# Performance work log

Hardware: AMD Instinct MI355X
Metric: run time of the kernel (lower is better)

The kernel has to match this reference:

```python
import jax, jax.numpy as jnp
import numpy as np

N, C, L, D, F = 8, 128, 512, 64, 512
ATTN_W = 64
LN_EPS = 1e-5
ATTN_EPS = 1e-6


def _xavier(k, shape):
    lim = float(np.sqrt(6.0 / (shape[0] + shape[1])))
    return jax.random.uniform(k, shape, jnp.float32, -lim, lim)


def setup_inputs() -> dict:
    key = jax.random.key(0)
    ks = jax.random.split(key, 8)
    return dict(
        x=jax.random.normal(ks[0], (N, C, L), jnp.float32),
        Wx=_xavier(ks[1], (C, D)),
        Wt=_xavier(ks[2], (C, D)),
        bh=jnp.zeros((D,), jnp.float32),
        Wa=_xavier(ks[3], (D, 1)),
        ba=jnp.zeros((1,), jnp.float32),
        W0=_xavier(ks[4], (C, F)),
        b0=jnp.zeros((F,), jnp.float32),
        W1=_xavier(ks[5], (F, C)),
        b1=jnp.zeros((C,), jnp.float32),
        g0=jnp.ones((C,), jnp.float32),
        be0=jnp.zeros((C,), jnp.float32),
        g1=jnp.ones((C,), jnp.float32),
        be1=jnp.zeros((C,), jnp.float32),
    )


def _layernorm(y, g, b):
    mu = jnp.mean(y, axis=-1, keepdims=True)
    var = jnp.var(y, axis=-1, keepdims=True)
    return (y - mu) * jax.lax.rsqrt(var + LN_EPS) * g + b


def reference(x, Wx, Wt, bh, Wa, ba, W0, b0, W1, b1, g0, be0, g1, be1):
    xt = jnp.transpose(x, (0, 2, 1))  # (N, L, C)
    q = jnp.einsum('nlc,cd->nld', xt, Wt)  # (N, L, D)
    k = jnp.einsum('nlc,cd->nld', xt, Wx)  # (N, L, D)
    # additive (Bahdanau) scores: h is the large (N, L, L, D) intermediate
    h = jnp.tanh(q[:, :, None, :] + k[:, None, :, :] + bh)
    e = jnp.einsum('nlmd,d->nlm', h, Wa[:, 0]) + ba[0]  # (N, L, L)
    e = jnp.exp(e - jnp.max(e, axis=-1, keepdims=True))
    # local band mask: tril(w//2 - 1) & triu(-w//2) on (row i, col j)
    dij = jnp.arange(L)[None, :] - jnp.arange(L)[:, None]  # j - i
    mask = (dij <= ATTN_W // 2 - 1) & (dij >= -(ATTN_W // 2))
    e = jnp.where(mask, e, 0.0)
    a = e / (jnp.sum(e, axis=-1, keepdims=True) + ATTN_EPS)  # (N, L, L)
    v = jnp.einsum('nlm,nmc->nlc', a, xt)  # (N, L, C)
    x2 = _layernorm(v + xt, g0, be0)
    x3 = jnp.einsum('nlf,fc->nlc', jax.nn.relu(jnp.einsum('nlc,cf->nlf', x2, W0) + b0), W1) + b1
    x4 = _layernorm(x3 + x2, g1, be1)
    return (jnp.transpose(x4, (0, 2, 1)), a)
```

## Files before the change

kernel.cpp:

```cpp
#include <hip/hip_runtime.h>
#include <cstddef>


__global__ __launch_bounds__(512) void prep_kernel(
    const float* __restrict__ x, const float* __restrict__ Wt,
    const float* __restrict__ Wx, float* __restrict__ q,
    float* __restrict__ k) {
  __shared__ float xs[128][17];
  int tid = threadIdx.x;
  int n = blockIdx.x >> 5;
  int l0 = (blockIdx.x & 31) << 4;

  {
    int c = tid >> 2, v = tid & 3;
    float4 d4 = *(const float4*)(x + ((size_t)n * 128 + c) * 512 + l0 + 4 * v);
    xs[c][4 * v + 0] = d4.x; xs[c][4 * v + 1] = d4.y;
    xs[c][4 * v + 2] = d4.z; xs[c][4 * v + 3] = d4.w;
  }
  __syncthreads();

  int half = tid >> 8;
  int t = tid & 255;
  int r = t >> 4;
  int f0 = (t & 15) << 2;
  const float* W = half ? Wx : Wt;
  float* dst = half ? k : q;
  float acc[4] = {0.f, 0.f, 0.f, 0.f};
#pragma unroll 4
  for (int cc = 0; cc < 128; cc++) {
    float xv = xs[cc][r];
    float4 w = *(const float4*)(W + cc * 64 + f0);
    acc[0] += xv * w.x; acc[1] += xv * w.y;
    acc[2] += xv * w.z; acc[3] += xv * w.w;
  }
  *(float4*)(dst + ((size_t)n * 512 + l0 + r) * 64 + f0) =
      make_float4(acc[0], acc[1], acc[2], acc[3]);
}

__global__ __launch_bounds__(512, 4) void attn_ffn_fused_kernel(
    const float* __restrict__ x, const float* __restrict__ q,
    const float* __restrict__ k, const float* __restrict__ bh,
    const float* __restrict__ Wa, const float* __restrict__ ba,
    const float* __restrict__ g0, const float* __restrict__ be0,
    const float* __restrict__ W0, const float* __restrict__ b0,
    const float* __restrict__ W1, const float* __restrict__ b1,
    const float* __restrict__ g1, const float* __restrict__ be1,
    float* __restrict__ a, float* __restrict__ out) {
  __shared__ __align__(16) char smem[61440];
  __shared__ __align__(16) float xstT[128][12];
  __shared__ __align__(16) float avT[71][10];
  __shared__ __align__(16) float was[64];

  float (*ks)[68] = (float(*)[68])smem;
  float (*qs)[64] = (float(*)[64])(smem + 19312);
  float (*xtw)[77] = (float(*)[77])(smem + 21360);
  float (*tstT)[12] = (float(*)[12])smem;
  float (*part)[8][128] = (float(*)[8][128])(smem + 24576);
  float (*ys)[128] = (float(*)[128])(smem + 57344);

  int tid = threadIdx.x;
  int w = tid >> 6, lane = tid & 63;
  int bid = blockIdx.x;
  int tile = (bid & 7) * 64 + (bid >> 3);
  size_t rbase = (size_t)tile * 8;
  int n = (int)(rbase >> 9);
  int i0 = (int)(rbase & 511);
  int jlo0 = i0 - 32;

  if (tid < 64) was[tid] = Wa[tid];
  for (int idx = tid; idx < 71 * 10; idx += 512) ((float*)avT)[idx] = 0.f;
  if (tid < 128) {
    int r = tid >> 4, d4 = (tid & 15) << 2;
    float4 qv = *(const float4*)(q + ((size_t)n * 512 + i0 + r) * 64 + d4);
    float4 bv = *(const float4*)(bh + d4);
    *(float4*)(&qs[r][d4]) =
        make_float4(qv.x + bv.x, qv.y + bv.y, qv.z + bv.z, qv.w + bv.w);
  }
  for (int idx = tid; idx < 71 * 16; idx += 512) {
    int row = idx >> 4, d4 = (idx & 15) << 2;
    int j = jlo0 + row;
    float4 v = make_float4(0.f, 0.f, 0.f, 0.f);
    if (j >= 0 && j < 512)
      v = *(const float4*)(k + ((size_t)n * 512 + j) * 64 + d4);
    *(float4*)(&ks[row][d4]) = v;
  }
  for (int t = tid; t < 128 * 18; t += 512) {
    int c = t / 18;
    int u = t - c * 18;
    int col = 4 * u;
    int j0 = jlo0 + col;
    const float* xp = x + ((size_t)n * 128 + c) * 512;
    float4 v = make_float4(0.f, 0.f, 0.f, 0.f);
    if (j0 >= 0 && j0 + 3 < 512) {
      v = *(const float4*)(xp + j0);
    } else {
      if (j0 + 0 >= 0 && j0 + 0 < 512) v.x = xp[j0 + 0];
      if (j0 + 1 >= 0 && j0 + 1 < 512) v.y = xp[j0 + 1];
      if (j0 + 2 >= 0 && j0 + 2 < 512) v.z = xp[j0 + 2];
      if (j0 + 3 >= 0 && j0 + 3 < 512) v.w = xp[j0 + 3];
    }
    xtw[c][col + 0] = v.x; xtw[c][col + 1] = v.y;
    xtw[c][col + 2] = v.z; xtw[c][col + 3] = v.w;
  }
  __syncthreads();

  {
    int r = w;
    int i = i0 + r;
    int j = jlo0 + r + lane;
    bool valid = (j >= 0 && j < 512);
    const float* krow = &ks[r + lane][0];
    float e = 0.f;
#pragma unroll
    for (int d4 = 0; d4 < 64; d4 += 4) {
      float4 kv = *(const float4*)(krow + d4);
      float4 qv = *(const float4*)(&qs[r][d4]);
      float4 wv = *(const float4*)(&was[d4]);
      float h0 = qv.x + kv.x, h1 = qv.y + kv.y;
      float h2 = qv.z + kv.z, h3 = qv.w + kv.w;
      float t0 = 1.f - 2.f * __builtin_amdgcn_rcpf(__expf(2.f * h0) + 1.f);
      float t1 = 1.f - 2.f * __builtin_amdgcn_rcpf(__expf(2.f * h1) + 1.f);
      float t2 = 1.f - 2.f * __builtin_amdgcn_rcpf(__expf(2.f * h2) + 1.f);
      float t3 = 1.f - 2.f * __builtin_amdgcn_rcpf(__expf(2.f * h3) + 1.f);
      e += wv.x * t0 + wv.y * t1 + wv.z * t2 + wv.w * t3;
    }
    e += ba[0];
    if (!valid) e = -1e30f;

    float m = e;
    for (int o = 32; o > 0; o >>= 1) m = fmaxf(m, __shfl_xor(m, o, 64));
    float ex = valid ? __expf(e - m) : 0.f;
    float s = ex;
    for (int o = 32; o > 0; o >>= 1) s += __shfl_xor(s, o, 64);
    avT[r + lane][r] = ex / (s + 1e-6f);

    float* arow = a + ((size_t)n * 512 + i) * 512;
    int jlo = i - 32;
#pragma unroll
    for (int t = 0; t < 2; t++) {
      int col0 = 4 * lane + 256 * t;
      float4 v;
      { int jr = col0 + 0 - jlo; int jc = min(max(jr, 0), 63); v.x = (jr >= 0 && jr < 64) ? avT[r + jc][r] : 0.f; }
      { int jr = col0 + 1 - jlo; int jc = min(max(jr, 0), 63); v.y = (jr >= 0 && jr < 64) ? avT[r + jc][r] : 0.f; }
      { int jr = col0 + 2 - jlo; int jc = min(max(jr, 0), 63); v.z = (jr >= 0 && jr < 64) ? avT[r + jc][r] : 0.f; }
      { int jr = col0 + 3 - jlo; int jc = min(max(jr, 0), 63); v.w = (jr >= 0 && jr < 64) ? avT[r + jc][r] : 0.f; }
      *(float4*)(arow + col0) = v;
    }
  }
  __syncthreads();

  {
    int c = tid & 127;
    int r0 = (tid >> 7) << 1;
    const float* xr = &xtw[c][0];
    float acc0 = 0.f, acc1 = 0.f;
#pragma unroll 5
    for (int m = 0; m < 65; m++) {
      int col = r0 + m;
      float xv = xr[col];
      float2 av2 = *(const float2*)(&avT[col][r0]);
      acc0 += av2.x * xv;
      acc1 += av2.y * xv;
    }
    float res0 = xr[32 + r0];
    float res1 = xr[33 + r0];
    *(float2*)(&xstT[c][r0]) = make_float2(acc0 + res0, acc1 + res1);
  }
  __syncthreads();

  {
    float a0 = xstT[lane][w], a1 = xstT[lane + 64][w];
    float s = a0 + a1, s2 = a0 * a0 + a1 * a1;
    for (int o = 32; o > 0; o >>= 1) {
      s += __shfl_xor(s, o, 64);
      s2 += __shfl_xor(s2, o, 64);
    }
    float mu = s * (1.f / 128.f);
    float var = s2 * (1.f / 128.f) - mu * mu;
    float rs = rsqrtf(var + 1e-5f);
    xstT[lane][w] = (a0 - mu) * rs * g0[lane] + be0[lane];
    xstT[lane + 64][w] = (a1 - mu) * rs * g0[lane + 64] + be0[lane + 64];
  }
  __syncthreads();

  {
    int g = lane & 15;
    int kq = lane >> 4;
    int f0 = (16 * w + g) << 2;
    int ccb = kq << 5;
    const float* w0p = W0 + (size_t)ccb * 512 + f0;
    float acc[8][4];
#pragma unroll
    for (int i = 0; i < 8; i++)
#pragma unroll
      for (int u = 0; u < 4; u++) acc[i][u] = 0.f;

    float4 wbuf[4];
#pragma unroll
    for (int p = 0; p < 4; p++)
      wbuf[p] = *(const float4*)(w0p + (size_t)p * 512);
#pragma unroll
    for (int c4 = 0; c4 < 8; c4++) {
      float4 cur0 = wbuf[0], cur1 = wbuf[1], cur2 = wbuf[2], cur3 = wbuf[3];
      if (c4 < 7) {
#pragma unroll
        for (int p = 0; p < 4; p++)
          wbuf[p] = *(const float4*)(w0p + (size_t)((c4 + 1) * 4 + p) * 512);
      }
#pragma unroll
      for (int p = 0; p < 4; p++) {
        int cc = ccb + c4 * 4 + p;
        float4 wv = (p == 0) ? cur0 : (p == 1) ? cur1 : (p == 2) ? cur2 : cur3;
        float4 xa = *(const float4*)(&xstT[cc][0]);
        float4 xb = *(const float4*)(&xstT[cc][4]);
        acc[0][0] += xa.x * wv.x; acc[0][1] += xa.x * wv.y; acc[0][2] += xa.x * wv.z; acc[0][3] += xa.x * wv.w;
        acc[1][0] += xa.y * wv.x; acc[1][1] += xa.y * wv.y; acc[1][2] += xa.y * wv.z; acc[1][3] += xa.y * wv.w;
        acc[2][0] += xa.z * wv.x; acc[2][1] += xa.z * wv.y; acc[2][2] += xa.z * wv.z; acc[2][3] += xa.z * wv.w;
        acc[3][0] += xa.w * wv.x; acc[3][1] += xa.w * wv.y; acc[3][2] += xa.w * wv.z; acc[3][3] += xa.w * wv.w;
        acc[4][0] += xb.x * wv.x; acc[4][1] += xb.x * wv.y; acc[4][2] += xb.x * wv.z; acc[4][3] += xb.x * wv.w;
        acc[5][0] += xb.y * wv.x; acc[5][1] += xb.y * wv.y; acc[5][2] += xb.y * wv.z; acc[5][3] += xb.y * wv.w;
        acc[6][0] += xb.z * wv.x; acc[6][1] += xb.z * wv.y; acc[6][2] += xb.z * wv.z; acc[6][3] += xb.z * wv.w;
        acc[7][0] += xb.w * wv.x; acc[7][1] += xb.w * wv.y; acc[7][2] += xb.w * wv.z; acc[7][3] += xb.w * wv.w;
      }
    }
#pragma unroll
    for (int i = 0; i < 8; i++)
#pragma unroll
      for (int u = 0; u < 4; u++) {
        float v = acc[i][u];
        v += __shfl_xor(v, 16, 64);
        v += __shfl_xor(v, 32, 64);
        acc[i][u] = v;
      }
    int f = f0 + kq;
    float bb = b0[f];
    float r0v[8];
#pragma unroll
    for (int i = 0; i < 8; i++) {
      float v = (kq == 0) ? acc[i][0] : (kq == 1) ? acc[i][1]
              : (kq == 2) ? acc[i][2] : acc[i][3];
      r0v[i] = fmaxf(v + bb, 0.f);
    }
    *(float4*)(&tstT[f][0]) = make_float4(r0v[0], r0v[1], r0v[2], r0v[3]);
    *(float4*)(&tstT[f][4]) = make_float4(r0v[4], r0v[5], r0v[6], r0v[7]);
  }
  __syncthreads();

  {
    int c0 = (lane & 31) << 2;
    int rh = lane >> 5;
    const float* W1p = W1 + (size_t)w * 64 * 128 + c0;
    int tb = w << 6;
    float acc[4][4];
#pragma unroll
    for (int i = 0; i < 4; i++)
#pragma unroll
      for (int u = 0; u < 4; u++) acc[i][u] = 0.f;

    float4 wbuf[4];
#pragma unroll
    for (int p = 0; p < 4; p++)
      wbuf[p] = *(const float4*)(W1p + (size_t)p * 128);
#pragma unroll
    for (int t4 = 0; t4 < 16; t4++) {
      float4 cur0 = wbuf[0], cur1 = wbuf[1], cur2 = wbuf[2], cur3 = wbuf[3];
      if (t4 < 15) {
#pragma unroll
        for (int p = 0; p < 4; p++)
          wbuf[p] = *(const float4*)(W1p + (size_t)((t4 + 1) * 4 + p) * 128);
      }
#pragma unroll
      for (int p = 0; p < 4; p++) {
        int t = t4 * 4 + p;
        float4 wv = (p == 0) ? cur0 : (p == 1) ? cur1 : (p == 2) ? cur2 : cur3;
        float4 tv = *(const float4*)(&tstT[tb + t][4 * rh]);
        acc[0][0] += tv.x * wv.x; acc[0][1] += tv.x * wv.y; acc[0][2] += tv.x * wv.z; acc[0][3] += tv.x * wv.w;
        acc[1][0] += tv.y * wv.x; acc[1][1] += tv.y * wv.y; acc[1][2] += tv.y * wv.z; acc[1][3] += tv.y * wv.w;
        acc[2][0] += tv.z * wv.x; acc[2][1] += tv.z * wv.y; acc[2][2] += tv.z * wv.z; acc[2][3] += tv.z * wv.w;
        acc[3][0] += tv.w * wv.x; acc[3][1] += tv.w * wv.y; acc[3][2] += tv.w * wv.z; acc[3][3] += tv.w * wv.w;
      }
    }
#pragma unroll
    for (int i = 0; i < 4; i++) {
      *(float4*)(&part[w][4 * rh + i][c0]) =
          make_float4(acc[i][0], acc[i][1], acc[i][2], acc[i][3]);
    }
  }
  __syncthreads();

  {
    float a0 = b1[lane] + xstT[lane][w];
    float a1 = b1[lane + 64] + xstT[lane + 64][w];
#pragma unroll
    for (int ko = 0; ko < 8; ko++) {
      a0 += part[ko][w][lane];
      a1 += part[ko][w][lane + 64];
    }
    float s = a0 + a1, s2 = a0 * a0 + a1 * a1;
    for (int o = 32; o > 0; o >>= 1) {
      s += __shfl_xor(s, o, 64);
      s2 += __shfl_xor(s2, o, 64);
    }
    float mu = s * (1.f / 128.f);
    float var = s2 * (1.f / 128.f) - mu * mu;
    float rs = rsqrtf(var + 1e-5f);
    ys[w][lane] = (a0 - mu) * rs * g1[lane] + be1[lane];
    ys[w][lane + 64] = (a1 - mu) * rs * g1[lane + 64] + be1[lane + 64];
  }
  __syncthreads();

  {
    int c = tid >> 2, tq = tid & 3;
    *(float2*)(out + ((size_t)n * 128 + c) * 512 + i0 + 2 * tq) =
        make_float2(ys[2 * tq][c], ys[2 * tq + 1][c]);
  }
}

extern "C" void kernel_launch(void* const* d_in, const int* in_sizes, int n_in,
                              void* d_out, int out_size, void* d_ws, size_t ws_size,
                              hipStream_t stream) {
  const float* x   = (const float*)d_in[0];
  const float* Wx  = (const float*)d_in[1];
  const float* Wt  = (const float*)d_in[2];
  const float* bh  = (const float*)d_in[3];
  const float* Wa  = (const float*)d_in[4];
  const float* ba  = (const float*)d_in[5];
  const float* W0  = (const float*)d_in[6];
  const float* b0  = (const float*)d_in[7];
  const float* W1  = (const float*)d_in[8];
  const float* b1  = (const float*)d_in[9];
  const float* g0  = (const float*)d_in[10];
  const float* be0 = (const float*)d_in[11];
  const float* g1  = (const float*)d_in[12];
  const float* be1 = (const float*)d_in[13];

  float* outx = (float*)d_out;
  float* outa = outx + (size_t)524288;

  float* ws = (float*)d_ws;
  float* q  = ws;
  float* k  = q + 262144;

  prep_kernel<<<256, 512, 0, stream>>>(x, Wt, Wx, q, k);
  attn_ffn_fused_kernel<<<512, 512, 0, stream>>>(
      x, q, k, bh, Wa, ba, g0, be0, W0, b0, W1, b1, g1, be1, outa, outx);
}
```

Before: 124.6 us.

## Shrink shared memory with fp16 x window and aliased buffers to raise occupancy

Stores the x window used for the attention-value product in fp16 and keeps the fp32 residual rows in a separate small buffer. The FFN partial-sum and output staging buffers now alias existing shared memory, with an extra barrier added before the overwrite. Together this cuts the shared allocation so the launch bound can allow 6 blocks per CU instead of 4. The cost is reduced precision in the a·x product, one more barrier, and avT padding changed from 10 to 9, which breaks the float2 loads.

Result: slower. 133.0 us (+6.7%).

```diff
diff --git a/kernel.cpp b/kernel.cpp
--- a/kernel.cpp
+++ b/kernel.cpp
@@ -1,4 +1,5 @@
 #include <hip/hip_runtime.h>
+#include <hip/hip_fp16.h>
 #include <cstddef>
 
 
@@ -37,7 +38,7 @@
       make_float4(acc[0], acc[1], acc[2], acc[3]);
 }
 
-__global__ __launch_bounds__(512, 4) void attn_ffn_fused_kernel(
+__global__ __launch_bounds__(512, 6) void attn_ffn_fused_kernel(
     const float* __restrict__ x, const float* __restrict__ q,
     const float* __restrict__ k, const float* __restrict__ bh,
     const float* __restrict__ Wa, const float* __restrict__ ba,
@@ -46,17 +47,17 @@
     const float* __restrict__ W1, const float* __restrict__ b1,
     const float* __restrict__ g1, const float* __restrict__ be1,
     float* __restrict__ a, float* __restrict__ out) {
-  __shared__ __align__(16) char smem[61440];
+  __shared__ __align__(16) char smem[45456];
   __shared__ __align__(16) float xstT[128][12];
-  __shared__ __align__(16) float avT[71][10];
-  __shared__ __align__(16) float was[64];
+  __shared__ float avT[71][9];
+  __shared__ float was[64];
 
   float (*ks)[68] = (float(*)[68])smem;
   float (*qs)[64] = (float(*)[64])(smem + 19312);
-  float (*xtw)[77] = (float(*)[77])(smem + 21360);
+  __half* xtw = (__half*)(smem + 21360);
+  float (*xres)[129] = (float(*)[129])(smem + 41328);
   float (*tstT)[12] = (float(*)[12])smem;
-  float (*part)[8][128] = (float(*)[8][128])(smem + 24576);
-  float (*ys)[128] = (float(*)[128])(smem + 57344);
+  float (*part)[8][128] = (float(*)[8][128])smem;
 
   int tid = threadIdx.x;
   int w = tid >> 6, lane = tid & 63;
@@ -68,7 +69,7 @@
   int jlo0 = i0 - 32;
 
   if (tid < 64) was[tid] = Wa[tid];
-  for (int idx = tid; idx < 71 * 10; idx += 512) ((float*)avT)[idx] = 0.f;
+  for (int idx = tid; idx < 71 * 9; idx += 512) ((float*)avT)[idx] = 0.f;
   if (tid < 128) {
     int r = tid >> 4, d4 = (tid & 15) << 2;
     float4 qv = *(const float4*)(q + ((size_t)n * 512 + i0 + r) * 64 + d4);
@@ -99,8 +100,16 @@
       if (j0 + 2 >= 0 && j0 + 2 < 512) v.z = xp[j0 + 2];
       if (j0 + 3 >= 0 && j0 + 3 < 512) v.w = xp[j0 + 3];
     }
-    xtw[c][col + 0] = v.x; xtw[c][col + 1] = v.y;
-    xtw[c][col + 2] = v.z; xtw[c][col + 3] = v.w;
+    __half2 p01, p23;
+    p01.x = __float2half(v.x); p01.y = __float2half(v.y);
+    p23.x = __float2half(v.z); p23.y = __float2half(v.w);
+    *(__half2*)(xtw + c * 78 + col) = p01;
+    *(__half2*)(xtw + c * 78 + col + 2) = p23;
+    if (u == 8 || u == 9) {
+      int r0x = col - 32;
+      xres[r0x + 0][c] = v.x; xres[r0x + 1][c] = v.y;
+      xres[r0x + 2][c] = v.z; xres[r0x + 3][c] = v.w;
+    }
   }
   __syncthreads();
 
@@ -152,18 +161,19 @@
   {
     int c = tid & 127;
     int r0 = (tid >> 7) << 1;
-    const float* xr = &xtw[c][0];
+    const __half* xr = xtw + c * 78;
     float acc0 = 0.f, acc1 = 0.f;
 #pragma unroll 5
     for (int m = 0; m < 65; m++) {
       int col = r0 + m;
-      float xv = xr[col];
-      float2 av2 = *(const float2*)(&avT[col][r0]);
-      acc0 += av2.x * xv;
-      acc1 += av2.y * xv;
-    }
-    float res0 = xr[32 + r0];
-    float res1 = xr[33 + r0];
+      float xv = __half2float(xr[col]);
+      float a0 = avT[col][r0];
+      float a1 = avT[col][r0 + 1];
+      acc0 += a0 * xv;
+      acc1 += a1 * xv;
+    }
+    float res0 = xres[r0][c];
+    float res1 = xres[r0 + 1][c];
     *(float2*)(&xstT[c][r0]) = make_float2(acc0 + res0, acc1 + res1);
   }
   __syncthreads();
@@ -246,16 +256,16 @@
   }
   __syncthreads();
 
+  float g2acc[4][4];
   {
     int c0 = (lane & 31) << 2;
     int rh = lane >> 5;
     const float* W1p = W1 + (size_t)w * 64 * 128 + c0;
     int tb = w << 6;
-    float acc[4][4];
 #pragma unroll
     for (int i = 0; i < 4; i++)
 #pragma unroll
-      for (int u = 0; u < 4; u++) acc[i][u] = 0.f;
+      for (int u = 0; u < 4; u++) g2acc[i][u] = 0.f;
 
     float4 wbuf[4];
 #pragma unroll
@@ -274,16 +284,22 @@
         int t = t4 * 4 + p;
         float4 wv = (p == 0) ? cur0 : (p == 1) ? cur1 : (p == 2) ? cur2 : cur3;
         float4 tv = *(const float4*)(&tstT[tb + t][4 * rh]);
-        acc[0][0] += tv.x * wv.x; acc[0][1] += tv.x * wv.y; acc[0][2] += tv.x * wv.z; acc[0][3] += tv.x * wv.w;
-        acc[1][0] += tv.y * wv.x; acc[1][1] += tv.y * wv.y; acc[1][2] += tv.y * wv.z; acc[1][3] += tv.y * wv.w;
-        acc[2][0] += tv.z * wv.x; acc[2][1] += tv.z * wv.y; acc[2][2] += tv.z * wv.z; acc[2][3] += tv.z * wv.w;
-        acc[3][0] += tv.w * wv.x; acc[3][1] += tv.w * wv.y; acc[3][2] += tv.w * wv.z; acc[3][3] += tv.w * wv.w;
-      }
-    }
+        g2acc[0][0] += tv.x * wv.x; g2acc[0][1] += tv.x * wv.y; g2acc[0][2] += tv.x * wv.z; g2acc[0][3] += tv.x * wv.w;
+        g2acc[1][0] += tv.y * wv.x; g2acc[1][1] += tv.y * wv.y; g2acc[1][2] += tv.y * wv.z; g2acc[1][3] += tv.y * wv.w;
+        g2acc[2][0] += tv.z * wv.x; g2acc[2][1] += tv.z * wv.y; g2acc[2][2] += tv.z * wv.z; g2acc[2][3] += tv.z * wv.w;
+        g2acc[3][0] += tv.w * wv.x; g2acc[3][1] += tv.w * wv.y; g2acc[3][2] += tv.w * wv.z; g2acc[3][3] += tv.w * wv.w;
+      }
+    }
+  }
+  __syncthreads();
+
+  {
+    int c0 = (lane & 31) << 2;
+    int rh = lane >> 5;
 #pragma unroll
     for (int i = 0; i < 4; i++) {
       *(float4*)(&part[w][4 * rh + i][c0]) =
-          make_float4(acc[i][0], acc[i][1], acc[i][2], acc[i][3]);
+          make_float4(g2acc[i][0], g2acc[i][1], g2acc[i][2], g2acc[i][3]);
     }
   }
   __syncthreads();
@@ -304,15 +320,15 @@
     float mu = s * (1.f / 128.f);
     float var = s2 * (1.f / 128.f) - mu * mu;
     float rs = rsqrtf(var + 1e-5f);
-    ys[w][lane] = (a0 - mu) * rs * g1[lane] + be1[lane];
-    ys[w][lane + 64] = (a1 - mu) * rs * g1[lane + 64] + be1[lane + 64];
+    xstT[lane][w] = (a0 - mu) * rs * g1[lane] + be1[lane];
+    xstT[lane + 64][w] = (a1 - mu) * rs * g1[lane + 64] + be1[lane + 64];
   }
   __syncthreads();
 
   {
     int c = tid >> 2, tq = tid & 3;
     *(float2*)(out + ((size_t)n * 128 + c) * 512 + i0 + 2 * tq) =
-        make_float2(ys[2 * tq][c], ys[2 * tq + 1][c]);
+        make_float2(xstT[c][2 * tq], xstT[c][2 * tq + 1]);
   }
 }
 
```
